# Kernel optimization log

Hardware: AMD Instinct MI355X
Metric: run time of the kernel (lower is better)

Reference implementation:

```python
import jax, jax.numpy as jnp
import numpy as np

D_MODEL = 1024
NHEAD = 16
NUM_KV = 4
D_K = D_MODEL // NHEAD          # 64
GROUP = NHEAD // NUM_KV          # 4 query heads per kv head
ROPE_BASE = 10000.0


def _rope(x, seq_len):
    """Apply rotary embedding. x: [B, h, S, d_k], positions 0..seq_len-1."""
    half = D_K // 2
    inv_freq = 1.0 / (ROPE_BASE ** (jnp.arange(0, D_K, 2, dtype=jnp.float32) / D_K))
    t = jnp.arange(seq_len, dtype=jnp.float32)
    freqs = jnp.outer(t, inv_freq)                      # [S, d_k/2]
    emb = jnp.concatenate([freqs, freqs], axis=-1)      # [S, d_k]
    cos, sin = jnp.cos(emb), jnp.sin(emb)               # broadcast over B, h
    x1, x2 = x[..., :half], x[..., half:]
    rot = jnp.concatenate([-x2, x1], axis=-1)
    return x * cos + rot * sin


def setup_inputs() -> dict:
    key = jax.random.key(0)
    ks = jax.random.split(key, 12)
    B, S = 2, 2048
    s_in = 1.0 / np.sqrt(D_MODEL)
    inp = {
        "query": jax.random.normal(ks[0], (B, S, D_MODEL), jnp.float32),
        "key":   jax.random.normal(ks[1], (B, S, D_MODEL), jnp.float32),
        "value": jax.random.normal(ks[2], (B, S, D_MODEL), jnp.float32),
        "Wq": jax.random.normal(ks[3], (D_MODEL, D_MODEL), jnp.float32) * s_in,
        "bq": jnp.zeros((D_MODEL,), jnp.float32),
        "Wk": jax.random.normal(ks[4], (NUM_KV * D_K, D_MODEL), jnp.float32) * s_in,
        "bk": jnp.zeros((NUM_KV * D_K,), jnp.float32),
        "Wv": jax.random.normal(ks[5], (NUM_KV * D_K, D_MODEL), jnp.float32) * s_in,
        "bv": jnp.zeros((NUM_KV * D_K,), jnp.float32),
        "Wo": jax.random.normal(ks[6], (D_MODEL, D_MODEL), jnp.float32) * s_in,
        "bo": jnp.zeros((D_MODEL,), jnp.float32),
    }
    return inp


def reference(query, key, value, Wq, bq, Wk, bk, Wv, bv, Wo, bo):
    B, S, _ = query.shape
    T = key.shape[1]
    # projections (torch Linear: x @ W^T + b)
    Q = (query @ Wq.T + bq).reshape(B, S, NHEAD, D_K).transpose(0, 2, 1, 3)   # [B,H,S,dk]
    K = (key   @ Wk.T + bk).reshape(B, T, NUM_KV, D_K).transpose(0, 2, 1, 3)  # [B,KV,T,dk]
    V = (value @ Wv.T + bv).reshape(B, T, NUM_KV, D_K).transpose(0, 2, 1, 3)
    # fused RoPE (start_pos = 0)
    Q = _rope(Q, S)
    K = _rope(K, T)
    # expand kv heads (repeat_interleave on head dim)
    Kr = jnp.repeat(K, GROUP, axis=1)   # [B,H,T,dk]
    Vr = jnp.repeat(V, GROUP, axis=1)
    scale = 1.0 / np.sqrt(D_K)
    scores = jnp.einsum("bhsd,bhtd->bhst", Q, Kr) * scale   # [B,H,S,T]
    attn = jax.nn.softmax(scores, axis=-1)                    # dropout = eval/no-op
    context = jnp.einsum("bhst,bhtd->bhsd", attn, Vr)        # [B,H,S,dk]
    context = context.transpose(0, 2, 1, 3).reshape(B, S, D_MODEL)
    return context @ Wo.T + bo
```

## Files before the change

kernel.cpp:

```cpp
#include <hip/hip_runtime.h>
#include <hip/hip_bf16.h>

typedef __hip_bfloat16 bf16;
typedef __attribute__((ext_vector_type(8))) short short8;
typedef __attribute__((ext_vector_type(4))) short short4v;
typedef __attribute__((ext_vector_type(4))) float f32x4;
typedef __attribute__((ext_vector_type(4))) float float4v;

static __device__ inline short f2bf(float f){
  __hip_bfloat16 h = __float2bfloat16(f);
  return *reinterpret_cast<short*>(&h);
}

static __device__ __forceinline__ unsigned cvt_pk_bf16(float lo, float hi){
  unsigned r;
  asm("v_cvt_pk_bf16_f32 %0, %1, %2" : "=v"(r) : "v"(lo), "v"(hi));
  return r;
}

static __device__ __forceinline__ float exp2_fast(float x){
  float r;
  asm("v_exp_f32 %0, %1" : "=v"(r) : "v"(x));
  return r;
}

static __device__ __forceinline__ float max3f(float a, float b, float c){
  float r;
  asm("v_max3_f32 %0, %1, %2, %3" : "=v"(r) : "v"(a), "v"(b), "v"(c));
  return r;
}

static __device__ inline short8 load8(const float* p){
  float4v a = *reinterpret_cast<const float4v*>(p);
  float4v b = *reinterpret_cast<const float4v*>(p + 4);
  short8 r;
  unsigned* u = reinterpret_cast<unsigned*>(&r);
  u[0] = cvt_pk_bf16(a[0], a[1]);
  u[1] = cvt_pk_bf16(a[2], a[3]);
  u[2] = cvt_pk_bf16(b[0], b[1]);
  u[3] = cvt_pk_bf16(b[2], b[3]);
  return r;
}
static __device__ inline short8 load8(const bf16* p){
  return *reinterpret_cast<const short8*>(p);
}

typedef __attribute__((address_space(1))) const unsigned int gas_u32;
typedef __attribute__((address_space(3))) unsigned int las_u32;
static __device__ __forceinline__ void gload16(const void* g, void* l){
  __builtin_amdgcn_global_load_lds((gas_u32*)g, (las_u32*)l, 16, 0, 0);
}

template<int N>
static __device__ __forceinline__ void vm_barrier(){
  if constexpr (N == 8) asm volatile("s_waitcnt vmcnt(8)" ::: "memory");
  else if constexpr (N == 4) asm volatile("s_waitcnt vmcnt(4)" ::: "memory");
  else asm volatile("s_waitcnt vmcnt(0)" ::: "memory");
  __builtin_amdgcn_s_barrier();
  __builtin_amdgcn_sched_barrier(0);
}

__global__ void rope_table_kernel(float* __restrict__ tab){
  const int idx = blockIdx.x * 256 + threadIdx.x;
  const int d = idx & 31, s = idx >> 5;
  const float ang = (float)s * exp2f(-0.41524101186092030f * (float)d);
  float sn, cs;
  sincosf(ang, &sn, &cs);
  tab[idx*2] = cs; tab[idx*2+1] = sn;
}

#define CVT_Q   0
#define CVT_K   4194304
#define CVT_V   8388608
#define CVT_WQ  12582912
#define CVT_WK  13631488
#define CVT_WV  13893632
#define CVT_WO  14155776
#define CVT_TOT 15204352
__global__ void cvt_kernel(bf16* __restrict__ dst,
    const float* q, const float* k, const float* v,
    const float* wq, const float* wk, const float* wv, const float* wo){
  const size_t i8 = ((size_t)blockIdx.x * 256 + threadIdx.x) * 8;
  const float* src; size_t off;
  if      (i8 < CVT_K ){ src = q;  off = i8; }
  else if (i8 < CVT_V ){ src = k;  off = i8 - CVT_K; }
  else if (i8 < CVT_WQ){ src = v;  off = i8 - CVT_V; }
  else if (i8 < CVT_WK){ src = wq; off = i8 - CVT_WQ; }
  else if (i8 < CVT_WV){ src = wk; off = i8 - CVT_WK; }
  else if (i8 < CVT_WO){ src = wv; off = i8 - CVT_WV; }
  else                 { src = wo; off = i8 - CVT_WO; }
  *reinterpret_cast<short8*>(reinterpret_cast<short*>(dst) + i8) = load8(src + off);
}

template<int MODE>
__device__ __forceinline__ void gemm_bt_v2(
    short* lds, void* __restrict__ Cout,
    const bf16* __restrict__ A, const bf16* __restrict__ B,
    const float* __restrict__ bias, const float* __restrict__ tab,
    int ntile, int N, int K)
{
  const int NK = K >> 5;
  const int n0 = ntile * 128, m0 = blockIdx.y * 128;
  const int tid = threadIdx.x, w = tid >> 6, lane = tid & 63;
  const int wm = w >> 1, wn = w & 1, lr = lane & 15, lg = lane >> 4;
  const int r0 = w*32 + (lane >> 2), r1 = r0 + 16;
  const int c0 = ((lane & 3) ^ ((r0 >> 1) & 3)) * 8;
  const int c1 = ((lane & 3) ^ ((r1 >> 1) & 3)) * 8;
  const bf16* A0 = A + (size_t)(m0 + r0) * K + c0;
  const bf16* A1 = A + (size_t)(m0 + r1) * K + c1;
  const bf16* B0 = B + (size_t)(n0 + r0) * K + c0;
  const bf16* B1 = B + (size_t)(n0 + r1) * K + c1;
  const int ldsW = (w*32) * 32;
  int offA[4], offB[4];
  #pragma unroll
  for (int i = 0; i < 4; i++){
    const int ra = wm*64 + i*16 + lr;
    offA[i] = ra*64 + ((lg ^ ((ra >> 1) & 3)) * 16);
    const int rb = wn*64 + i*16 + lr;
    offB[i] = rb*64 + ((lg ^ ((rb >> 1) & 3)) * 16);
  }
  auto stage = [&](int t){
    short* bufA = lds + (t & 3) * 8192;
    short* bufB = bufA + 4096;
    gload16(A0 + t*32, bufA + ldsW);
    gload16(A1 + t*32, bufA + ldsW + 512);
    gload16(B0 + t*32, bufB + ldsW);
    gload16(B1 + t*32, bufB + ldsW + 512);
  };
  f32x4 acc[4][4] = {};
  stage(0); stage(1);
  for (int t = 0; t < NK; t++){
    if (t + 2 < NK){ stage(t + 2); vm_barrier<8>(); }
    else if (t + 1 < NK){ vm_barrier<4>(); }
    else { vm_barrier<0>(); }
    const char* bufA = (const char*)(lds + (t & 3) * 8192);
    const char* bufB = bufA + 8192;
    short8 af[4], bfm[4];
    #pragma unroll
    for (int mt = 0; mt < 4; mt++) af[mt]  = *(const short8*)(bufA + offA[mt]);
    #pragma unroll
    for (int nt = 0; nt < 4; nt++) bfm[nt] = *(const short8*)(bufB + offB[nt]);
    __builtin_amdgcn_s_setprio(1);
    #pragma unroll
    for (int mt = 0; mt < 4; mt++)
      #pragma unroll
      for (int nt = 0; nt < 4; nt++)
        acc[mt][nt] = __builtin_amdgcn_mfma_f32_16x16x32_bf16(af[mt], bfm[nt], acc[mt][nt], 0, 0, 0);
    __builtin_amdgcn_s_setprio(0);
  }
  if constexpr (MODE == 0){
    float* C = (float*)Cout;
    #pragma unroll
    for (int mt = 0; mt < 4; mt++){
      #pragma unroll
      for (int nt = 0; nt < 4; nt++){
        const int col = n0 + wn*64 + nt*16 + lr;
        const float bv = bias[col];
        const int rbase = m0 + wm*64 + mt*16 + lg*4;
        #pragma unroll
        for (int i = 0; i < 4; i++)
          C[(size_t)(rbase + i) * N + col] = acc[mt][nt][i] + bv;
      }
    }
  } else if constexpr (MODE == 1 || MODE == 2){
    bf16* dst = (bf16*)Cout;
    constexpr int NH = (MODE == 1) ? 16 : 4;
    constexpr float SC = (MODE == 1) ? 0.18033688011112042f : 1.0f;
    #pragma unroll
    for (int mt = 0; mt < 4; mt++){
      #pragma unroll
      for (int nt = 0; nt < 2; nt++){
        const int col = n0 + wn*64 + nt*16 + lr;
        const int d = col & 63;
        const int hh = col >> 6;
        const float b1 = bias[col], b2 = bias[col + 32];
        #pragma unroll
        for (int i = 0; i < 4; i++){
          const int m = m0 + wm*64 + mt*16 + lg*4 + i;
          const int s = m & 2047, bb = m >> 11;
          const float cs = tab[(s*32 + d)*2], sn = tab[(s*32 + d)*2 + 1];
          const float x1 = acc[mt][nt][i] + b1;
          const float x2 = acc[mt][nt+2][i] + b2;
          const size_t o = ((size_t)(bb*NH + hh) * 2048 + s) * 64 + d;
          dst[o]      = __float2bfloat16((x1*cs - x2*sn) * SC);
          dst[o + 32] = __float2bfloat16((x2*cs + x1*sn) * SC);
        }
      }
    }
  } else {
    bf16* dst = (bf16*)Cout;
    #pragma unroll
    for (int mt = 0; mt < 4; mt++){
      #pragma unroll
      for (int nt = 0; nt < 4; nt++){
        const int col = n0 + wn*64 + nt*16 + lr;
        const int kv = col >> 6, d = col & 63;
        const float bv = bias[col];
        #pragma unroll
        for (int i = 0; i < 4; i++){
          const int m = m0 + wm*64 + mt*16 + lg*4 + i;
          const int s = m & 2047, bb = m >> 11;
          dst[((size_t)(bb*4 + kv) * 64 + d) * 2048 + s] = __float2bfloat16(acc[mt][nt][i] + bv);
        }
      }
    }
  }
}

__global__ __launch_bounds__(256) void gemm_qkv_kernel(
    bf16* Qa, bf16* Ka, bf16* Va, const bf16* cvt,
    const float* bq, const float* bk, const float* bv, const float* tab){
  __shared__ short lds[4 * 8192];
  const int x = blockIdx.x;
  if (x < 8)
    gemm_bt_v2<1>(lds, Qa, cvt + CVT_Q, cvt + CVT_WQ, bq, tab, x,    1024, 1024);
  else if (x < 10)
    gemm_bt_v2<2>(lds, Ka, cvt + CVT_K, cvt + CVT_WK, bk, tab, x-8,  256, 1024);
  else
    gemm_bt_v2<3>(lds, Va, cvt + CVT_V, cvt + CVT_WV, bv, tab, x-10, 256, 1024);
}
__global__ __launch_bounds__(256) void gemm_out_kernel(
    float* C, const bf16* ctx, const bf16* cvt, const float* bo){
  __shared__ short lds[4 * 8192];
  gemm_bt_v2<0>(lds, C, ctx, cvt + CVT_WO, bo, nullptr, blockIdx.x, 1024, 1024);
}

__global__ __launch_bounds__(256) void attn_kernel(
    bf16* __restrict__ ctx, const bf16* __restrict__ Qa,
    const bf16* __restrict__ Ka, const bf16* __restrict__ Vt)
{
  __shared__ short Klds[4][64 * 64];
  __shared__ short Vlds[4][64 * 64];
  const int bh = blockIdx.y, b = bh >> 4, h = bh & 15, kvh = h >> 2;
  const int q0 = blockIdx.x * 128;
  const int tid = threadIdx.x, w = tid >> 6, lane = tid & 63;
  const int lr = lane & 15, lg = lane >> 4;
  const bf16* Qbase = Qa + (size_t)bh * 2048 * 64;
  const bf16* Kbase = Ka + (size_t)(b*4 + kvh) * 2048 * 64;
  const bf16* Vbase = Vt + (size_t)(b*4 + kvh) * 64 * 2048;

  short8 qf[2][2];
  #pragma unroll
  for (int qt = 0; qt < 2; qt++){
    qf[qt][0] = load8(Qbase + (size_t)(q0 + w*32 + qt*16 + lr) * 64 + lg*8);
    qf[qt][1] = load8(Qbase + (size_t)(q0 + w*32 + qt*16 + lr) * 64 + 32 + lg*8);
  }

  const int l8 = lane >> 3;
  const int ch = (lane & 7) ^ l8;
  const bf16* kSrc = Kbase + (size_t)(w*16 + l8) * 64 + ch*8;
  const bf16* vSrc = Vbase + (size_t)(w*16 + l8) * 2048 + ch*8;
  auto stage = [&](int bi, int t){
    short* Kd = &Klds[bi][(w*16) * 64];
    short* Vd = &Vlds[bi][(w*16) * 64];
    const bf16* ks = kSrc + (size_t)t * 64 * 64;
    const bf16* vs = vSrc + t * 64;
    gload16(ks,           Kd);
    gload16(ks + 8*64,    Kd + 8*64);
    gload16(vs,           Vd);
    gload16(vs + 8*2048,  Vd + 8*64);
  };

  float mrow[2] = {-1e30f, -1e30f}, lsum[2] = {0.f, 0.f};
  f32x4 o[2][4] = {};

  auto swzb = [](int row, int cb) -> int { return row*128 + (cb ^ ((row & 7) << 4)); };

  auto qk = [&](const char* Kc, f32x4 (&st)[4][2]){
    __builtin_amdgcn_s_setprio(1);
    #pragma unroll
    for (int mt = 0; mt < 4; mt++){
      short8 kf0 = *reinterpret_cast<const short8*>(Kc + swzb(mt*16 + lr, lg*16));
      short8 kf1 = *reinterpret_cast<const short8*>(Kc + swzb(mt*16 + lr, 64 + lg*16));
      #pragma unroll
      for (int qt = 0; qt < 2; qt++){
        st[mt][qt] = __builtin_amdgcn_mfma_f32_16x16x32_bf16(kf0, qf[qt][0], (f32x4){0.f,0.f,0.f,0.f}, 0, 0, 0);
        st[mt][qt] = __builtin_amdgcn_mfma_f32_16x16x32_bf16(kf1, qf[qt][1], st[mt][qt], 0, 0, 0);
      }
    }
    __builtin_amdgcn_s_setprio(0);
  };

  auto softmax_pv = [&](f32x4 (&st)[4][2], const char* Vc){
    short8 pf[2][2];
    #pragma unroll
    for (int qt = 0; qt < 2; qt++){
      float mx = max3f(st[0][qt][0], st[0][qt][1], st[0][qt][2]);
      mx = max3f(mx, st[0][qt][3], st[1][qt][0]);
      mx = max3f(mx, st[1][qt][1], st[1][qt][2]);
      mx = max3f(mx, st[1][qt][3], st[2][qt][0]);
      mx = max3f(mx, st[2][qt][1], st[2][qt][2]);
      mx = max3f(mx, st[2][qt][3], st[3][qt][0]);
      mx = max3f(mx, st[3][qt][1], st[3][qt][2]);
      mx = fmaxf(mx, st[3][qt][3]);
      if (__any(mx > mrow[qt] + 8.0f)){
        mx = fmaxf(mx, __shfl_xor(mx, 16));
        mx = fmaxf(mx, __shfl_xor(mx, 32));
        const float nm = fmaxf(mrow[qt], mx);
        const float alpha = exp2_fast(mrow[qt] - nm);
        mrow[qt] = nm;
        lsum[qt] *= alpha;
        float ab[4];
        #pragma unroll
        for (int i = 0; i < 4; i++) ab[i] = __shfl(alpha, lg*4 + i);
        #pragma unroll
        for (int dt = 0; dt < 4; dt++)
          #pragma unroll
          for (int i = 0; i < 4; i++)
            o[qt][dt][i] *= ab[i];
      }
      float s = 0.f;
      unsigned* pw = reinterpret_cast<unsigned*>(&pf[qt][0]);
      #pragma unroll
      for (int j = 0; j < 8; j++){
        const int mt = j >> 1, i0 = (j & 1) * 2;
        const float e0 = exp2_fast(st[mt][qt][i0]     - mrow[qt]);
        const float e1 = exp2_fast(st[mt][qt][i0 + 1] - mrow[qt]);
        pw[j] = cvt_pk_bf16(e0, e1);
        s += e0 + e1;
      }
      lsum[qt] += s;
    }
    __builtin_amdgcn_s_setprio(1);
    #pragma unroll
    for (int dt = 0; dt < 4; dt++){
      #pragma unroll
      for (int kkA = 0; kkA < 2; kkA++){
        short8 vf;
        *reinterpret_cast<short4v*>(&vf) =
            *reinterpret_cast<const short4v*>(Vc + swzb(dt*16 + lr, kkA*64 + lg*8));
        *reinterpret_cast<short4v*>(reinterpret_cast<short*>(&vf) + 4) =
            *reinterpret_cast<const short4v*>(Vc + swzb(dt*16 + lr, kkA*64 + lg*8 + 32));
        #pragma unroll
        for (int qt = 0; qt < 2; qt++)
          o[qt][dt] = __builtin_amdgcn_mfma_f32_16x16x32_bf16(pf[qt][kkA], vf, o[qt][dt], 0, 0, 0);
      }
    }
    __builtin_amdgcn_s_setprio(0);
  };

  f32x4 stA[4][2], stB[4][2];

  stage(0, 0); stage(1, 1);
  vm_barrier<4>();
  qk((const char*)&Klds[0][0], stA);

  for (int tt = 0; tt < 32; tt += 2){
    if (tt + 2 < 32){ stage((tt+2) & 3, tt+2); vm_barrier<4>(); }
    else vm_barrier<0>();
    qk((const char*)&Klds[(tt+1) & 3][0], stB);
    softmax_pv(stA, (const char*)&Vlds[tt & 3][0]);
    if (tt + 3 < 32){ stage((tt+3) & 3, tt+3); vm_barrier<4>(); }
    else vm_barrier<0>();
    if (tt + 2 < 32) qk((const char*)&Klds[(tt+2) & 3][0], stA);
    softmax_pv(stB, (const char*)&Vlds[(tt+1) & 3][0]);
  }

  #pragma unroll
  for (int qt = 0; qt < 2; qt++){
    float s = lsum[qt];
    s += __shfl_xor(s, 16);
    s += __shfl_xor(s, 32);
    float lb[4];
    #pragma unroll
    for (int i = 0; i < 4; i++) lb[i] = 1.0f / __shfl(s, lg*4 + i);
    #pragma unroll
    for (int dt = 0; dt < 4; dt++){
      #pragma unroll
      for (int i = 0; i < 4; i++){
        const int q = q0 + w*32 + qt*16 + lg*4 + i;
        ctx[(size_t)(b*2048 + q) * 1024 + h*64 + dt*16 + lr] =
            __float2bfloat16(o[qt][dt][i] * lb[i]);
      }
    }
  }
}

extern "C" void kernel_launch(void* const* d_in, const int* in_sizes, int n_in,
                              void* d_out, int out_size, void* d_ws, size_t ws_size,
                              hipStream_t stream)
{
  const float* query = (const float*)d_in[0];
  const float* key   = (const float*)d_in[1];
  const float* value = (const float*)d_in[2];
  const float* Wq = (const float*)d_in[3];
  const float* bq = (const float*)d_in[4];
  const float* Wk = (const float*)d_in[5];
  const float* bk = (const float*)d_in[6];
  const float* Wv = (const float*)d_in[7];
  const float* bv = (const float*)d_in[8];
  const float* Wo = (const float*)d_in[9];
  const float* bo = (const float*)d_in[10];
  float* out = (float*)d_out;

  char* ws = (char*)d_ws;
  size_t off = 0;
  float* tab = (float*)(ws + off); off += (size_t)2048 * 32 * 2 * 4;
  bf16*  Qa  = (bf16*)(ws + off);  off += (size_t)32 * 2048 * 64 * 2;
  bf16*  Ka  = (bf16*)(ws + off);  off += (size_t)8 * 2048 * 64 * 2;
  bf16*  Va  = (bf16*)(ws + off);  off += (size_t)8 * 64 * 2048 * 2;
  bf16*  ctx = (bf16*)(ws + off);  off += (size_t)2 * 2048 * 1024 * 2;
  bf16*  cvt = (bf16*)(ws + off);  off += (size_t)CVT_TOT * 2;

  rope_table_kernel<<<256, 256, 0, stream>>>(tab);
  cvt_kernel<<<CVT_TOT / 8 / 256, 256, 0, stream>>>(cvt, query, key, value, Wq, Wk, Wv, Wo);
  gemm_qkv_kernel<<<dim3(12, 32), 256, 0, stream>>>(Qa, Ka, Va, cvt, bq, bk, bv, tab);
  attn_kernel<<<dim3(16, 32), 256, 0, stream>>>(ctx, Qa, Ka, Va);
  gemm_out_kernel<<<dim3(8, 32), 256, 0, stream>>>(out, ctx, cvt, bo);
}
```

Baseline: 120.4 us.

## Use 8 waves per attention block and fold rope table into cvt kernel

After: 124.4 us. +3.4%, slower.

```diff
diff --git a/kernel.cpp b/kernel.cpp
--- a/kernel.cpp
+++ b/kernel.cpp
@@ -55,18 +55,10 @@
 static __device__ __forceinline__ void vm_barrier(){
   if constexpr (N == 8) asm volatile("s_waitcnt vmcnt(8)" ::: "memory");
   else if constexpr (N == 4) asm volatile("s_waitcnt vmcnt(4)" ::: "memory");
+  else if constexpr (N == 2) asm volatile("s_waitcnt vmcnt(2)" ::: "memory");
   else asm volatile("s_waitcnt vmcnt(0)" ::: "memory");
   __builtin_amdgcn_s_barrier();
   __builtin_amdgcn_sched_barrier(0);
-}
-
-__global__ void rope_table_kernel(float* __restrict__ tab){
-  const int idx = blockIdx.x * 256 + threadIdx.x;
-  const int d = idx & 31, s = idx >> 5;
-  const float ang = (float)s * exp2f(-0.41524101186092030f * (float)d);
-  float sn, cs;
-  sincosf(ang, &sn, &cs);
-  tab[idx*2] = cs; tab[idx*2+1] = sn;
 }
 
 #define CVT_Q   0
@@ -77,9 +69,17 @@
 #define CVT_WV  13893632
 #define CVT_WO  14155776
 #define CVT_TOT 15204352
-__global__ void cvt_kernel(bf16* __restrict__ dst,
+__global__ void cvt_kernel(bf16* __restrict__ dst, float* __restrict__ tab,
     const float* q, const float* k, const float* v,
     const float* wq, const float* wk, const float* wv, const float* wo){
+  if (blockIdx.x < 256){
+    const int idx = blockIdx.x * 256 + threadIdx.x;
+    const int d = idx & 31, s = idx >> 5;
+    const float ang = (float)s * exp2f(-0.41524101186092030f * (float)d);
+    float sn, cs;
+    sincosf(ang, &sn, &cs);
+    tab[idx*2] = cs; tab[idx*2+1] = sn;
+  }
   const size_t i8 = ((size_t)blockIdx.x * 256 + threadIdx.x) * 8;
   const float* src; size_t off;
   if      (i8 < CVT_K ){ src = q;  off = i8; }
@@ -225,7 +225,7 @@
   gemm_bt_v2<0>(lds, C, ctx, cvt + CVT_WO, bo, nullptr, blockIdx.x, 1024, 1024);
 }
 
-__global__ __launch_bounds__(256) void attn_kernel(
+__global__ __launch_bounds__(512) void attn_kernel(
     bf16* __restrict__ ctx, const bf16* __restrict__ Qa,
     const bf16* __restrict__ Ka, const bf16* __restrict__ Vt)
 {
@@ -239,67 +239,54 @@
   const bf16* Kbase = Ka + (size_t)(b*4 + kvh) * 2048 * 64;
   const bf16* Vbase = Vt + (size_t)(b*4 + kvh) * 64 * 2048;
 
-  short8 qf[2][2];
-  #pragma unroll
-  for (int qt = 0; qt < 2; qt++){
-    qf[qt][0] = load8(Qbase + (size_t)(q0 + w*32 + qt*16 + lr) * 64 + lg*8);
-    qf[qt][1] = load8(Qbase + (size_t)(q0 + w*32 + qt*16 + lr) * 64 + 32 + lg*8);
-  }
+  short8 qf[2];
+  qf[0] = load8(Qbase + (size_t)(q0 + w*16 + lr) * 64 + lg*8);
+  qf[1] = load8(Qbase + (size_t)(q0 + w*16 + lr) * 64 + 32 + lg*8);
 
   const int l8 = lane >> 3;
   const int ch = (lane & 7) ^ l8;
-  const bf16* kSrc = Kbase + (size_t)(w*16 + l8) * 64 + ch*8;
-  const bf16* vSrc = Vbase + (size_t)(w*16 + l8) * 2048 + ch*8;
+  const bf16* kSrc = Kbase + (size_t)(w*8 + l8) * 64 + ch*8;
+  const bf16* vSrc = Vbase + (size_t)(w*8 + l8) * 2048 + ch*8;
   auto stage = [&](int bi, int t){
-    short* Kd = &Klds[bi][(w*16) * 64];
-    short* Vd = &Vlds[bi][(w*16) * 64];
-    const bf16* ks = kSrc + (size_t)t * 64 * 64;
-    const bf16* vs = vSrc + t * 64;
-    gload16(ks,           Kd);
-    gload16(ks + 8*64,    Kd + 8*64);
-    gload16(vs,           Vd);
-    gload16(vs + 8*2048,  Vd + 8*64);
+    gload16(kSrc + (size_t)t * 64 * 64, &Klds[bi][(w*8) * 64]);
+    gload16(vSrc + t * 64,              &Vlds[bi][(w*8) * 64]);
   };
 
-  float mrow[2] = {-1e30f, -1e30f}, lsum[2] = {0.f, 0.f};
-  f32x4 o[2][4] = {};
+  float mrow = -1e30f, lsum = 0.f;
+  f32x4 o[4] = {};
 
   auto swzb = [](int row, int cb) -> int { return row*128 + (cb ^ ((row & 7) << 4)); };
 
-  auto qk = [&](const char* Kc, f32x4 (&st)[4][2]){
+  auto qk = [&](const char* Kc, f32x4 (&st)[4]){
     __builtin_amdgcn_s_setprio(1);
     #pragma unroll
     for (int mt = 0; mt < 4; mt++){
       short8 kf0 = *reinterpret_cast<const short8*>(Kc + swzb(mt*16 + lr, lg*16));
       short8 kf1 = *reinterpret_cast<const short8*>(Kc + swzb(mt*16 + lr, 64 + lg*16));
-      #pragma unroll
-      for (int qt = 0; qt < 2; qt++){
-        st[mt][qt] = __builtin_amdgcn_mfma_f32_16x16x32_bf16(kf0, qf[qt][0], (f32x4){0.f,0.f,0.f,0.f}, 0, 0, 0);
-        st[mt][qt] = __builtin_amdgcn_mfma_f32_16x16x32_bf16(kf1, qf[qt][1], st[mt][qt], 0, 0, 0);
-      }
+      st[mt] = __builtin_amdgcn_mfma_f32_16x16x32_bf16(kf0, qf[0], (f32x4){0.f,0.f,0.f,0.f}, 0, 0, 0);
+      st[mt] = __builtin_amdgcn_mfma_f32_16x16x32_bf16(kf1, qf[1], st[mt], 0, 0, 0);
     }
     __builtin_amdgcn_s_setprio(0);
   };
 
-  auto softmax_pv = [&](f32x4 (&st)[4][2], const char* Vc){
-    short8 pf[2][2];
-    #pragma unroll
-    for (int qt = 0; qt < 2; qt++){
-      float mx = max3f(st[0][qt][0], st[0][qt][1], st[0][qt][2]);
-      mx = max3f(mx, st[0][qt][3], st[1][qt][0]);
-      mx = max3f(mx, st[1][qt][1], st[1][qt][2]);
-      mx = max3f(mx, st[1][qt][3], st[2][qt][0]);
-      mx = max3f(mx, st[2][qt][1], st[2][qt][2]);
-      mx = max3f(mx, st[2][qt][3], st[3][qt][0]);
-      mx = max3f(mx, st[3][qt][1], st[3][qt][2]);
-      mx = fmaxf(mx, st[3][qt][3]);
-      if (__any(mx > mrow[qt] + 8.0f)){
+  auto softmax_pv = [&](f32x4 (&st)[4], const char* Vc){
+    short8 pf[2];
+    {
+      float mx = max3f(st[0][0], st[0][1], st[0][2]);
+      mx = max3f(mx, st[0][3], st[1][0]);
+      mx = max3f(mx, st[1][1], st[1][2]);
+      mx = max3f(mx, st[1][3], st[2][0]);
+      mx = max3f(mx, st[2][1], st[2][2]);
+      mx = max3f(mx, st[2][3], st[3][0]);
+      mx = max3f(mx, st[3][1], st[3][2]);
+      mx = fmaxf(mx, st[3][3]);
+      if (__any(mx > mrow + 8.0f)){
         mx = fmaxf(mx, __shfl_xor(mx, 16));
         mx = fmaxf(mx, __shfl_xor(mx, 32));
-        const float nm = fmaxf(mrow[qt], mx);
-        const float alpha = exp2_fast(mrow[qt] - nm);
-        mrow[qt] = nm;
-        lsum[qt] *= alpha;
+        const float nm = fmaxf(mrow, mx);
+        const float alpha = exp2_fast(mrow - nm);
+        mrow = nm;
+        lsum *= alpha;
         float ab[4];
         #pragma unroll
         for (int i = 0; i < 4; i++) ab[i] = __shfl(alpha, lg*4 + i);
@@ -307,19 +294,19 @@
         for (int dt = 0; dt < 4; dt++)
           #pragma unroll
           for (int i = 0; i < 4; i++)
-            o[qt][dt][i] *= ab[i];
+            o[dt][i] *= ab[i];
       }
       float s = 0.f;
-      unsigned* pw = reinterpret_cast<unsigned*>(&pf[qt][0]);
+      unsigned* pw = reinterpret_cast<unsigned*>(&pf[0]);
       #pragma unroll
       for (int j = 0; j < 8; j++){
         const int mt = j >> 1, i0 = (j & 1) * 2;
-        const float e0 = exp2_fast(st[mt][qt][i0]     - mrow[qt]);
-        const float e1 = exp2_fast(st[mt][qt][i0 + 1] - mrow[qt]);
+        const float e0 = exp2_fast(st[mt][i0]     - mrow);
+        const float e1 = exp2_fast(st[mt][i0 + 1] - mrow);
         pw[j] = cvt_pk_bf16(e0, e1);
         s += e0 + e1;
       }
-      lsum[qt] += s;
+      lsum += s;
     }
     __builtin_amdgcn_s_setprio(1);
     #pragma unroll
@@ -331,34 +318,31 @@
             *reinterpret_cast<const short4v*>(Vc + swzb(dt*16 + lr, kkA*64 + lg*8));
         *reinterpret_cast<short4v*>(reinterpret_cast<short*>(&vf) + 4) =
             *reinterpret_cast<const short4v*>(Vc + swzb(dt*16 + lr, kkA*64 + lg*8 + 32));
-        #pragma unroll
-        for (int qt = 0; qt < 2; qt++)
-          o[qt][dt] = __builtin_amdgcn_mfma_f32_16x16x32_bf16(pf[qt][kkA], vf, o[qt][dt], 0, 0, 0);
+        o[dt] = __builtin_amdgcn_mfma_f32_16x16x32_bf16(pf[kkA], vf, o[dt], 0, 0, 0);
       }
     }
     __builtin_amdgcn_s_setprio(0);
   };
 
-  f32x4 stA[4][2], stB[4][2];
+  f32x4 stA[4], stB[4];
 
   stage(0, 0); stage(1, 1);
-  vm_barrier<4>();
+  vm_barrier<2>();
   qk((const char*)&Klds[0][0], stA);
 
   for (int tt = 0; tt < 32; tt += 2){
-    if (tt + 2 < 32){ stage((tt+2) & 3, tt+2); vm_barrier<4>(); }
+    if (tt + 2 < 32){ stage((tt+2) & 3, tt+2); vm_barrier<2>(); }
     else vm_barrier<0>();
     qk((const char*)&Klds[(tt+1) & 3][0], stB);
     softmax_pv(stA, (const char*)&Vlds[tt & 3][0]);
-    if (tt + 3 < 32){ stage((tt+3) & 3, tt+3); vm_barrier<4>(); }
+    if (tt + 3 < 32){ stage((tt+3) & 3, tt+3); vm_barrier<2>(); }
     else vm_barrier<0>();
     if (tt + 2 < 32) qk((const char*)&Klds[(tt+2) & 3][0], stA);
     softmax_pv(stB, (const char*)&Vlds[(tt+1) & 3][0]);
   }
 
-  #pragma unroll
-  for (int qt = 0; qt < 2; qt++){
-    float s = lsum[qt];
+  {
+    float s = lsum;
     s += __shfl_xor(s, 16);
     s += __shfl_xor(s, 32);
     float lb[4];
@@ -368,9 +352,9 @@
     for (int dt = 0; dt < 4; dt++){
       #pragma unroll
       for (int i = 0; i < 4; i++){
-        const int q = q0 + w*32 + qt*16 + lg*4 + i;
+        const int q = q0 + w*16 + lg*4 + i;
         ctx[(size_t)(b*2048 + q) * 1024 + h*64 + dt*16 + lr] =
-            __float2bfloat16(o[qt][dt][i] * lb[i]);
+            __float2bfloat16(o[dt][i] * lb[i]);
       }
     }
   }
@@ -402,9 +386,8 @@
   bf16*  ctx = (bf16*)(ws + off);  off += (size_t)2 * 2048 * 1024 * 2;
   bf16*  cvt = (bf16*)(ws + off);  off += (size_t)CVT_TOT * 2;
 
-  rope_table_kernel<<<256, 256, 0, stream>>>(tab);
-  cvt_kernel<<<CVT_TOT / 8 / 256, 256, 0, stream>>>(cvt, query, key, value, Wq, Wk, Wv, Wo);
+  cvt_kernel<<<CVT_TOT / 8 / 256, 256, 0, stream>>>(cvt, tab, query, key, value, Wq, Wk, Wv, Wo);
   gemm_qkv_kernel<<<dim3(12, 32), 256, 0, stream>>>(Qa, Ka, Va, cvt, bq, bk, bv, tab);
-  attn_kernel<<<dim3(16, 32), 256, 0, stream>>>(ctx, Qa, Ka, Va);
+  attn_kernel<<<dim3(16, 32), 512, 0, stream>>>(ctx, Qa, Ka, Va);
   gemm_out_kernel<<<dim3(8, 32), 256, 0, stream>>>(out, ctx, cvt, bo);
 }
```
